# Optimization experiments

Hardware: AMD Instinct MI355X
Metric: run time of the kernel (lower is better)

## Reference

```python
import jax, jax.numpy as jnp
import numpy as np

ITERATIONS = 20  # Resonator(iterations=20)
B, F, V, D = 128, 4, 2048, 4096


def _hardsign(x):
    # bipolar normalization used by MAP-VSA multiset(normalize=True); ties -> +1
    return jnp.where(x >= 0, 1.0, -1.0).astype(x.dtype)


def setup_inputs() -> dict:
    key = jax.random.key(0)
    k1, k2 = jax.random.split(key, 2)
    # bipolar codebooks: (F, V, D)
    codebooks = _hardsign(jax.random.normal(k1, (F, V, D), dtype=jnp.float32))
    # a realistic composite input: bind (elementwise product) of one codevector per factor
    idx = jax.random.randint(k2, (B, F), 0, V)                       # (B, F)
    chosen = codebooks[jnp.arange(F)[None, :], idx]                  # (B, F, D)
    inputs = jnp.prod(chosen, axis=1)                                # (B, D)
    # standard resonator init: normalized superposition of each codebook
    init_estimates = jnp.broadcast_to(
        _hardsign(jnp.sum(codebooks, axis=1)), (B, F, D)
    ).astype(jnp.float32)                                            # (B, F, D)
    return {"inputs": inputs, "init_estimates": init_estimates, "codebooks": codebooks}


def _resonator_step(inputs, est, codebooks):
    # est: (B, F, D). rolled stack over k=1..F-1 -> (B, F, F-1, D)
    f = est.shape[-2]
    rolled = jnp.stack([jnp.roll(est, k, axis=-2) for k in range(1, f)], axis=-2)
    inv_others = jnp.prod(rolled, axis=-2)          # multibind over dim -2 -> (B, F, D)
    new_est = inputs[:, None, :] * inv_others       # bind -> (B, F, D)
    sim = jnp.einsum('bfd,fvd->bfv', new_est, codebooks)   # similarity (activation='NONE')
    # multiset(codebooks, sim, normalize=True)
    return _hardsign(jnp.einsum('bfv,fvd->bfd', sim, codebooks))


def reference(inputs, init_estimates, codebooks):
    def body(carry, i):
        est, k, done = carry
        new = _resonator_step(inputs, est, codebooks)
        eq = jnp.all(new == est)          # convergence check (fixed point)
        k = jnp.where(done, k, i)
        return (new, k, done | eq), None

    carry0 = (init_estimates, jnp.int32(0), jnp.bool_(False))
    (est, k, _), _ = jax.lax.scan(body, carry0, jnp.arange(ITERATIONS, dtype=jnp.int32))
    # cleanup: argmax of |similarity| per factor (argmax_abs=True)
    sim = jnp.einsum('bfd,fvd->bfv', est, codebooks)
    outcome = jnp.argmax(jnp.abs(sim), axis=-1)     # (B, F) int indices
    return outcome, k
```

## Files before the change

### kernel.cpp

```cpp
#include <hip/hip_runtime.h>
#include <stdint.h>

#define B_    128
#define F_    4
#define V_    2048
#define D_    4096
#define DW    64
#define VW    32
#define ITERS 20
#define NKT   16
#define NBLK  512
#define ESLOT (B_ * F_ * DW)
#define SSLOT ((size_t)F_ * B_ * V_)

typedef _Float16 half8 __attribute__((ext_vector_type(8)));
typedef float   floatx4 __attribute__((ext_vector_type(4)));

__device__ __forceinline__ void cstore64(uint64_t* p, uint64_t v) {
    __hip_atomic_store(p, v, __ATOMIC_RELAXED, __HIP_MEMORY_SCOPE_AGENT);
}
__device__ __forceinline__ void cstore32(uint32_t* p, uint32_t v) {
    __hip_atomic_store(p, v, __ATOMIC_RELAXED, __HIP_MEMORY_SCOPE_AGENT);
}

__device__ __forceinline__ void xbar(int* bar, int gen) {
    __syncthreads();
    if (threadIdx.x == 0) {
        int s = blockIdx.x & 15;
        int t = __hip_atomic_fetch_add(&bar[s * 16], 1, __ATOMIC_RELAXED,
                                       __HIP_MEMORY_SCOPE_AGENT);
        if (t == gen * (NBLK / 16) - 1)
            __hip_atomic_fetch_add(&bar[256], 1, __ATOMIC_RELAXED,
                                   __HIP_MEMORY_SCOPE_AGENT);
        int spins = 0;
        while (__hip_atomic_load(&bar[256], __ATOMIC_RELAXED,
                                 __HIP_MEMORY_SCOPE_AGENT) < gen * 16) {
            __builtin_amdgcn_s_sleep(2);
            if (++spins > (1 << 16)) break;
        }
    }
    __syncthreads();
}

__device__ __forceinline__ void pack16(const float* __restrict__ x,
                                       uint64_t* __restrict__ bits, int t) {
    const float4* p = (const float4*)x + (size_t)t * 4;
    uint32_t m = 0;
    #pragma unroll
    for (int j = 0; j < 4; ++j) {
        float4 v = p[j];
        m |= (__float_as_uint(v.x) >> 31) << (4 * j + 0);
        m |= (__float_as_uint(v.y) >> 31) << (4 * j + 1);
        m |= (__float_as_uint(v.z) >> 31) << (4 * j + 2);
        m |= (__float_as_uint(v.w) >> 31) << (4 * j + 3);
    }
    ((unsigned short*)bits)[t] = (unsigned short)m;
}

__global__ __launch_bounds__(256) void k_setup(
        const float* __restrict__ cb, const float* __restrict__ inite,
        const float* __restrict__ inputs,
        uint64_t* __restrict__ cb_bits, uint64_t* __restrict__ est0,
        uint64_t* __restrict__ in_bits,
        int* __restrict__ flags, int* __restrict__ keys) {
    int gtid = blockIdx.x * 256 + threadIdx.x;
    const int T = 512 * 256;
    const int ncb = (F_ * V_ * D_) / 16;
    for (int t = gtid; t < ncb; t += T) pack16(cb, cb_bits, t);
    pack16(inite, est0, gtid);
    if (gtid < (B_ * D_) / 16) pack16(inputs, in_bits, gtid);
    if (gtid < 32) flags[gtid] = 0;
    if (gtid < B_ * F_) keys[gtid] = 0;
}

__global__ void k_packT(const uint64_t* __restrict__ cb_bits,
                        uint64_t* __restrict__ cbT) {
    int vw = blockIdx.x, dwg = blockIdx.y, f = blockIdx.z;
    int lane = threadIdx.x & 63;
    int dw = dwg * 4 + (threadIdx.x >> 6);
    uint64_t w = cb_bits[((size_t)f * V_ + vw * 64 + lane) * DW + dw];
    uint64_t r = 0;
    for (int d2 = 0; d2 < 64; ++d2) {
        uint64_t m = __ballot((unsigned)((w >> d2) & 1));
        if (lane == d2) r = m;
    }
    cbT[((size_t)f * D_ + dw * 64 + lane) * VW + vw] = r;
}

__global__ __launch_bounds__(256, 2) void k_loop(
        const uint64_t* __restrict__ cb_bits, const uint64_t* __restrict__ cbT,
        uint64_t* __restrict__ est_base, const uint64_t* __restrict__ in_bits,
        _Float16* __restrict__ simf_base, int* __restrict__ flags, int* bar) {
    const int bid = blockIdx.x;
    const int tid = threadIdx.x;
    int g = 0;

    __shared__ __align__(16) unsigned char LDSU[49152];
    __shared__ int bd;

    #pragma unroll 1
    for (int i = 0; i < ITERS; ++i) {
        const uint64_t* esti = est_base + (size_t)i * ESLOT;
        uint64_t*       esto = est_base + (size_t)(i + 1) * ESLOT;
        _Float16*       simf = simf_base + (size_t)i * SSLOT;

        {
            int vt = bid & 31, bt = (bid >> 5) & 3, f = bid >> 7;
            int v0 = vt * 64, b0 = bt * 32;
            ulonglong2* CB2 = (ulonglong2*)LDSU;
            ulonglong2* NB2 = (ulonglong2*)(LDSU + 32768);
            #pragma unroll
            for (int it = 0; it < 8; ++it) {
                int cq = it * 256 + tid;
                int r = cq >> 5, ch = cq & 31;
                const ulonglong2* src = (const ulonglong2*)(cb_bits + ((size_t)f * V_ + v0 + r) * DW);
                CB2[r * 32 + (ch ^ (r & 7))] = src[ch];
            }
            #pragma unroll
            for (int it = 0; it < 4; ++it) {
                int cq = it * 256 + tid;
                int r = cq >> 5, ch = cq & 31;
                int b = b0 + r;
                const ulonglong2* iv = (const ulonglong2*)(in_bits + (size_t)b * DW);
                const uint64_t* eb = esti + (size_t)b * F_ * DW;
                ulonglong2 i2 = iv[ch];
                ulonglong2 e0 = ((const ulonglong2*)(eb + 0 * DW))[ch];
                ulonglong2 e1 = ((const ulonglong2*)(eb + 1 * DW))[ch];
                ulonglong2 e2 = ((const ulonglong2*)(eb + 2 * DW))[ch];
                ulonglong2 e3 = ((const ulonglong2*)(eb + 3 * DW))[ch];
                uint64_t ex = (f == 0) ? e0.x : (f == 1) ? e1.x : (f == 2) ? e2.x : e3.x;
                uint64_t ey = (f == 0) ? e0.y : (f == 1) ? e1.y : (f == 2) ? e2.y : e3.y;
                ulonglong2 val;
                val.x = i2.x ^ e0.x ^ e1.x ^ e2.x ^ e3.x ^ ex;
                val.y = i2.y ^ e0.y ^ e1.y ^ e2.y ^ e3.y ^ ey;
                NB2[r * 32 + (ch ^ (r & 7))] = val;
            }
            __syncthreads();

            int vv = tid & 15, bb = tid >> 4;
            int svz = vv & 7, sbz = bb & 7;
            int pc[2][4];
            #pragma unroll
            for (int j = 0; j < 2; ++j)
                #pragma unroll
                for (int ii = 0; ii < 4; ++ii) pc[j][ii] = 0;

            #pragma unroll 4
            for (int ch = 0; ch < 32; ++ch) {
                ulonglong2 c[4], n[2];
                #pragma unroll
                for (int ii = 0; ii < 4; ++ii)
                    c[ii] = CB2[(vv + 16 * ii) * 32 + (ch ^ svz)];
                #pragma unroll
                for (int j = 0; j < 2; ++j)
                    n[j] = NB2[(bb + 16 * j) * 32 + (ch ^ sbz)];
                #pragma unroll
                for (int j = 0; j < 2; ++j)
                    #pragma unroll
                    for (int ii = 0; ii < 4; ++ii)
                        pc[j][ii] += __popcll(n[j].x ^ c[ii].x) + __popcll(n[j].y ^ c[ii].y);
            }
            #pragma unroll
            for (int j = 0; j < 2; ++j) {
                int b = b0 + bb + 16 * j;
                #pragma unroll
                for (int ii = 0; ii < 4; ++ii) {
                    int v = v0 + vv + 16 * ii;
                    union { _Float16 hf; unsigned short us; } cv;
                    cv.hf = (_Float16)(2048 - pc[j][ii]);
                    int other = __shfl_xor((int)cv.us, 1, 64);
                    if (!(vv & 1)) {
                        uint32_t packv = (uint32_t)cv.us | ((uint32_t)other << 16);
                        cstore32((uint32_t*)&simf[((size_t)f * B_ + b) * V_ + v], packv);
                    }
                }
            }
        }
        xbar(bar, ++g);

        {
            int gnt = bid & 63, gmt = (bid >> 6) & 1, gf = bid >> 7;
            int m0 = gmt * 64, n0 = gnt * 64;
            int lane = tid & 63, wave = tid >> 6;
            int lrow = lane & 15, lq = lane >> 4;
            int wm = wave & 1, wn = wave >> 1;

            uint64_t* Bb = (uint64_t*)LDSU;
            _Float16* As = (_Float16*)(LDSU + 16384);
            if (tid == 0) bd = 0;

            const uint64_t* bsrc = cbT + ((size_t)gf * D_ + n0) * VW;
            #pragma unroll
            for (int p = 0; p < 4; ++p) {
                int chunk = p * 256 + tid;
                int dloc = chunk >> 4, cw = chunk & 15;
                ulonglong2 val = *(const ulonglong2*)&bsrc[dloc * VW + cw * 2];
                *(ulonglong2*)&Bb[dloc * VW + ((cw ^ (dloc & 15)) * 2)] = val;
            }

            const _Float16* Ab = simf + (size_t)gf * B_ * V_ + (size_t)m0 * V_;
            int arow = tid >> 4, acol = tid & 15;
            half8 areg[4];
            #pragma unroll
            for (int p = 0; p < 4; ++p)
                areg[p] = *(const half8*)&Ab[(size_t)(p * 16 + arow) * V_ + acol * 8];

            floatx4 acc[2][2] = {};

            const uint64_t SPREAD = 0x1000200040008000ull;
            const uint64_t SMASK  = 0x8000800080008000ull;
            const uint64_t PONE   = 0x3C003C003C003C00ull;

            #pragma unroll 1
            for (int kt = 0; kt < NKT; ++kt) {
                __syncthreads();
                #pragma unroll
                for (int p = 0; p < 4; ++p)
                    *(half8*)&As[(p * 16 + arow) * 128 + ((acol ^ arow) * 8)] = areg[p];
                if (kt + 1 < NKT) {
                    #pragma unroll
                    for (int p = 0; p < 4; ++p)
                        areg[p] = *(const half8*)&Ab[(size_t)(p * 16 + arow) * V_ + (kt + 1) * 128 + acol * 8];
                }
                __syncthreads();

                ulonglong2 bw[2];
                #pragma unroll
                for (int nt2 = 0; nt2 < 2; ++nt2) {
                    int dloc = wn * 32 + nt2 * 16 + lrow;
                    bw[nt2] = *(const ulonglong2*)&Bb[dloc * VW + ((kt ^ (dloc & 15)) * 2)];
                }
                #pragma unroll
                for (int ks = 0; ks < 4; ++ks) {
                    half8 af[2];
                    #pragma unroll
                    for (int mt2 = 0; mt2 < 2; ++mt2) {
                        int row = wm * 32 + mt2 * 16 + lrow;
                        af[mt2] = *(const half8*)&As[row * 128 + (((ks * 4 + lq) ^ lrow) * 8)];
                    }
                    half8 bfrag[2];
                    #pragma unroll
                    for (int nt2 = 0; nt2 < 2; ++nt2) {
                        uint64_t w = (ks < 2) ? bw[nt2].x : bw[nt2].y;
                        uint32_t byte = (uint32_t)(w >> ((((ks & 1) * 4 + lq)) * 8)) & 0xFFu;
                        union { uint64_t q[2]; half8 h; } bu;
                        bu.q[0] = (((uint64_t)(byte & 0xFu) * SPREAD) & SMASK) ^ PONE;
                        bu.q[1] = (((uint64_t)(byte >> 4)   * SPREAD) & SMASK) ^ PONE;
                        bfrag[nt2] = bu.h;
                    }
                    #pragma unroll
                    for (int mt2 = 0; mt2 < 2; ++mt2)
                        #pragma unroll
                        for (int nt2 = 0; nt2 < 2; ++nt2)
                            acc[mt2][nt2] = __builtin_amdgcn_mfma_f32_16x16x32_f16(
                                af[mt2], bfrag[nt2], acc[mt2][nt2], 0, 0, 0);
                }
            }

            __syncthreads();
            unsigned char* S = (unsigned char*)As;
            #pragma unroll
            for (int mt2 = 0; mt2 < 2; ++mt2)
                #pragma unroll
                for (int nt2 = 0; nt2 < 2; ++nt2)
                    #pragma unroll
                    for (int r = 0; r < 4; ++r) {
                        int row = wm * 32 + mt2 * 16 + lq * 4 + r;
                        int col = wn * 32 + nt2 * 16 + lrow;
                        S[row * 64 + col] = (acc[mt2][nt2][r] < 0.0f) ? 1 : 0;
                    }
            __syncthreads();
            if (tid < 64) {
                const uint64_t* Sw = (const uint64_t*)S;
                uint64_t m = 0;
                #pragma unroll
                for (int j = 0; j < 8; ++j) {
                    uint64_t w = Sw[tid * 8 + j];
                    m |= ((w * 0x0102040810204080ull) >> 56) << (8 * j);
                }
                size_t widx = ((size_t)(m0 + tid) * F_ + gf) * DW + gnt;
                uint64_t old = esti[widx];
                cstore64(&esto[widx], m);
                if (old != m) atomicOr(&bd, 1);
            }
            __syncthreads();
            if (tid == 0 && bd) atomicOr(&flags[i], 1);
        }
        if (i + 1 < ITERS) xbar(bar, ++g);
    }
}

__global__ __launch_bounds__(256) void k_argmax(
        const uint64_t* __restrict__ cb_bits,
        const uint64_t* __restrict__ est_bits,
        int* __restrict__ keys) {
    int vt = blockIdx.x, f = blockIdx.y;
    int v0 = vt * 32;
    int tid = threadIdx.x;

    __shared__ __align__(16) ulonglong2 EB2[128 * 32];
    __shared__ __align__(16) ulonglong2 CBa[32 * 32];

    #pragma unroll
    for (int it = 0; it < 16; ++it) {
        int cq = it * 256 + tid;
        int r = cq >> 5, ch = cq & 31;
        const ulonglong2* src = (const ulonglong2*)(est_bits + ((size_t)r * F_ + f) * DW);
        EB2[r * 32 + (ch ^ (r & 7))] = src[ch];
    }
    #pragma unroll
    for (int it = 0; it < 4; ++it) {
        int cq = it * 256 + tid;
        int r = cq >> 5, ch = cq & 31;
        const ulonglong2* src = (const ulonglong2*)(cb_bits + ((size_t)f * V_ + v0 + r) * DW);
        CBa[r * 32 + (ch ^ (r & 7))] = src[ch];
    }
    __syncthreads();

    int vv = tid & 15, bb = tid >> 4;
    int svz = vv & 7, sbz = bb & 7;
    int pc[8][2];
    #pragma unroll
    for (int j = 0; j < 8; ++j) { pc[j][0] = 0; pc[j][1] = 0; }

    #pragma unroll 4
    for (int ch = 0; ch < 32; ++ch) {
        ulonglong2 c[2], n[8];
        #pragma unroll
        for (int i = 0; i < 2; ++i)
            c[i] = CBa[(vv + 16 * i) * 32 + (ch ^ svz)];
        #pragma unroll
        for (int j = 0; j < 8; ++j)
            n[j] = EB2[(bb + 16 * j) * 32 + (ch ^ sbz)];
        #pragma unroll
        for (int j = 0; j < 8; ++j)
            #pragma unroll
            for (int i = 0; i < 2; ++i)
                pc[j][i] += __popcll(n[j].x ^ c[i].x) + __popcll(n[j].y ^ c[i].y);
    }

    #pragma unroll
    for (int j = 0; j < 8; ++j) {
        int kj = (int)0x80000000;
        #pragma unroll
        for (int i = 0; i < 2; ++i) {
            int v = v0 + vv + 16 * i;
            int m = 2048 - pc[j][i]; if (m < 0) m = -m;
            int key = (m << 11) | (2047 - v);
            if (key > kj) kj = key;
        }
        #pragma unroll
        for (int s = 1; s < 16; s <<= 1) {
            int o = __shfl_xor(kj, s, 64);
            if (o > kj) kj = o;
        }
        if ((tid & 15) == 0)
            atomicMax(&keys[(size_t)(bb + 16 * j) * F_ + f], kj);
    }
}

__global__ void k_final(const int* __restrict__ keys, const int* __restrict__ flags,
                        int* __restrict__ out) {
    int tid = blockIdx.x * blockDim.x + threadIdx.x;
    if (tid < B_ * F_) out[tid] = 2047 - (keys[tid] & 0x7FF);
    if (tid == 0) {
        int k = ITERS - 1;
        for (int i = 0; i < ITERS; ++i) if (flags[i] == 0) { k = i; break; }
        out[B_ * F_] = k;
    }
}

extern "C" void kernel_launch(void* const* d_in, const int* in_sizes, int n_in,
                              void* d_out, int out_size, void* d_ws, size_t ws_size,
                              hipStream_t stream) {
    const float* inputs = (const float*)d_in[0];
    const float* inite  = (const float*)d_in[1];
    const float* cb     = (const float*)d_in[2];
    int* out = (int*)d_out;

    char* ws = (char*)d_ws;
    uint64_t* cb_bits  = (uint64_t*)ws;  ws += (size_t)F_ * V_ * DW * 8;
    uint64_t* cbT_bits = (uint64_t*)ws;  ws += (size_t)F_ * D_ * VW * 8;
    uint64_t* est_base = (uint64_t*)ws;  ws += (size_t)(ITERS + 1) * ESLOT * 8;
    uint64_t* in_bits  = (uint64_t*)ws;  ws += (size_t)B_ * DW * 8;
    _Float16* simf     = (_Float16*)ws;  ws += (size_t)ITERS * SSLOT * 2;
    int*      flags    = (int*)ws;       ws += 32 * 4;
    int*      keys     = (int*)ws;       ws += B_ * F_ * 4;
    int*      bar      = (int*)ws;       ws += 2048;

    hipMemsetAsync(bar, 0, 2048, stream);

    k_setup<<<512, 256, 0, stream>>>(cb, inite, inputs, cb_bits, est_base,
                                     in_bits, flags, keys);
    k_packT<<<dim3(32, 16, 4), 256, 0, stream>>>(cb_bits, cbT_bits);
    k_loop<<<NBLK, 256, 0, stream>>>(cb_bits, cbT_bits, est_base, in_bits,
                                     simf, flags, bar);
    k_argmax<<<dim3(64, 4), 256, 0, stream>>>(cb_bits,
                                              est_base + (size_t)ITERS * ESLOT, keys);
    k_final<<<2, 256, 0, stream>>>(keys, flags, out);
}
```

Measured before the change: 924.5 us.

## Keep codebook tiles resident in LDS across iterations and remap block indices

Loads each block's similarity-phase codebook tile and transposed-codebook GEMM tile into LDS once before the iteration loop instead of reloading them every iteration. LDS grows to 64 KB so both tiles stay resident alongside the per-iteration buffers. Block-to-tile mapping is also reshuffled so the low bits of the block index spread across factor and batch tiles, which changes which XCD/L2 each tile lands on. The larger LDS footprint may reduce occupancy below two blocks per CU.

Result: faster. 902.1 us (-2.4%).

```diff
diff --git a/kernel.cpp b/kernel.cpp
--- a/kernel.cpp
+++ b/kernel.cpp
@@ -95,8 +95,47 @@
     const int tid = threadIdx.x;
     int g = 0;
 
-    __shared__ __align__(16) unsigned char LDSU[49152];
+    __shared__ __align__(16) unsigned char LDSU[65536];
     __shared__ int bd;
+
+    const int sgrp = bid & 7;
+    const int s_bt = sgrp & 3, s_fhi = sgrp >> 2;
+    const int shi  = bid >> 3;
+    const int s_vt = shi & 31, s_flo = shi >> 5;
+    const int s_f  = s_fhi + 2 * s_flo;
+    const int s_v0 = s_vt * 64, s_b0 = s_bt * 32;
+
+    const int ggrp = bid & 7;
+    const int g_mt = ggrp & 1, g_f = ggrp >> 1;
+    const int g_nt = bid >> 3;
+    const int g_m0 = g_mt * 64, g_n0 = g_nt * 64;
+
+    ulonglong2* CB2 = (ulonglong2*)LDSU;
+    ulonglong2* NB2 = (ulonglong2*)(LDSU + 32768);
+    _Float16*   As  = (_Float16*)(LDSU + 32768);
+    uint64_t*   Bb  = (uint64_t*)(LDSU + 49152);
+
+    #pragma unroll
+    for (int it = 0; it < 8; ++it) {
+        int cq = it * 256 + tid;
+        int r = cq >> 5, ch = cq & 31;
+        const ulonglong2* src = (const ulonglong2*)(cb_bits + ((size_t)s_f * V_ + s_v0 + r) * DW);
+        CB2[r * 32 + (ch ^ (r & 7))] = src[ch];
+    }
+    {
+        const uint64_t* bsrc = cbT + ((size_t)g_f * D_ + g_n0) * VW;
+        #pragma unroll
+        for (int p = 0; p < 4; ++p) {
+            int chunk = p * 256 + tid;
+            int dloc = chunk >> 4, cw = chunk & 15;
+            ulonglong2 val = *(const ulonglong2*)&bsrc[dloc * VW + cw * 2];
+            *(ulonglong2*)&Bb[dloc * VW + ((cw ^ (dloc & 15)) * 2)] = val;
+        }
+    }
+
+    const uint64_t SPREAD = 0x1000200040008000ull;
+    const uint64_t SMASK  = 0x8000800080008000ull;
+    const uint64_t PONE   = 0x3C003C003C003C00ull;
 
     #pragma unroll 1
     for (int i = 0; i < ITERS; ++i) {
@@ -105,22 +144,11 @@
         _Float16*       simf = simf_base + (size_t)i * SSLOT;
 
         {
-            int vt = bid & 31, bt = (bid >> 5) & 3, f = bid >> 7;
-            int v0 = vt * 64, b0 = bt * 32;
-            ulonglong2* CB2 = (ulonglong2*)LDSU;
-            ulonglong2* NB2 = (ulonglong2*)(LDSU + 32768);
-            #pragma unroll
-            for (int it = 0; it < 8; ++it) {
-                int cq = it * 256 + tid;
-                int r = cq >> 5, ch = cq & 31;
-                const ulonglong2* src = (const ulonglong2*)(cb_bits + ((size_t)f * V_ + v0 + r) * DW);
-                CB2[r * 32 + (ch ^ (r & 7))] = src[ch];
-            }
             #pragma unroll
             for (int it = 0; it < 4; ++it) {
                 int cq = it * 256 + tid;
                 int r = cq >> 5, ch = cq & 31;
-                int b = b0 + r;
+                int b = s_b0 + r;
                 const ulonglong2* iv = (const ulonglong2*)(in_bits + (size_t)b * DW);
                 const uint64_t* eb = esti + (size_t)b * F_ * DW;
                 ulonglong2 i2 = iv[ch];
@@ -128,8 +156,8 @@
                 ulonglong2 e1 = ((const ulonglong2*)(eb + 1 * DW))[ch];
                 ulonglong2 e2 = ((const ulonglong2*)(eb + 2 * DW))[ch];
                 ulonglong2 e3 = ((const ulonglong2*)(eb + 3 * DW))[ch];
-                uint64_t ex = (f == 0) ? e0.x : (f == 1) ? e1.x : (f == 2) ? e2.x : e3.x;
-                uint64_t ey = (f == 0) ? e0.y : (f == 1) ? e1.y : (f == 2) ? e2.y : e3.y;
+                uint64_t ex = (s_f == 0) ? e0.x : (s_f == 1) ? e1.x : (s_f == 2) ? e2.x : e3.x;
+                uint64_t ey = (s_f == 0) ? e0.y : (s_f == 1) ? e1.y : (s_f == 2) ? e2.y : e3.y;
                 ulonglong2 val;
                 val.x = i2.x ^ e0.x ^ e1.x ^ e2.x ^ e3.x ^ ex;
                 val.y = i2.y ^ e0.y ^ e1.y ^ e2.y ^ e3.y ^ ey;
@@ -162,16 +190,16 @@
             }
             #pragma unroll
             for (int j = 0; j < 2; ++j) {
-                int b = b0 + bb + 16 * j;
+                int b = s_b0 + bb + 16 * j;
                 #pragma unroll
                 for (int ii = 0; ii < 4; ++ii) {
-                    int v = v0 + vv + 16 * ii;
+                    int v = s_v0 + vv + 16 * ii;
                     union { _Float16 hf; unsigned short us; } cv;
                     cv.hf = (_Float16)(2048 - pc[j][ii]);
                     int other = __shfl_xor((int)cv.us, 1, 64);
                     if (!(vv & 1)) {
                         uint32_t packv = (uint32_t)cv.us | ((uint32_t)other << 16);
-                        cstore32((uint32_t*)&simf[((size_t)f * B_ + b) * V_ + v], packv);
+                        cstore32((uint32_t*)&simf[((size_t)s_f * B_ + b) * V_ + v], packv);
                     }
                 }
             }
@@ -179,26 +207,12 @@
         xbar(bar, ++g);
 
         {
-            int gnt = bid & 63, gmt = (bid >> 6) & 1, gf = bid >> 7;
-            int m0 = gmt * 64, n0 = gnt * 64;
             int lane = tid & 63, wave = tid >> 6;
             int lrow = lane & 15, lq = lane >> 4;
             int wm = wave & 1, wn = wave >> 1;
-
-            uint64_t* Bb = (uint64_t*)LDSU;
-            _Float16* As = (_Float16*)(LDSU + 16384);
             if (tid == 0) bd = 0;
 
-            const uint64_t* bsrc = cbT + ((size_t)gf * D_ + n0) * VW;
-            #pragma unroll
-            for (int p = 0; p < 4; ++p) {
-                int chunk = p * 256 + tid;
-                int dloc = chunk >> 4, cw = chunk & 15;
-                ulonglong2 val = *(const ulonglong2*)&bsrc[dloc * VW + cw * 2];
-                *(ulonglong2*)&Bb[dloc * VW + ((cw ^ (dloc & 15)) * 2)] = val;
-            }
-
-            const _Float16* Ab = simf + (size_t)gf * B_ * V_ + (size_t)m0 * V_;
+            const _Float16* Ab = simf + (size_t)g_f * B_ * V_ + (size_t)g_m0 * V_;
             int arow = tid >> 4, acol = tid & 15;
             half8 areg[4];
             #pragma unroll
@@ -206,10 +220,6 @@
                 areg[p] = *(const half8*)&Ab[(size_t)(p * 16 + arow) * V_ + acol * 8];
 
             floatx4 acc[2][2] = {};
-
-            const uint64_t SPREAD = 0x1000200040008000ull;
-            const uint64_t SMASK  = 0x8000800080008000ull;
-            const uint64_t PONE   = 0x3C003C003C003C00ull;
 
             #pragma unroll 1
             for (int kt = 0; kt < NKT; ++kt) {
@@ -278,7 +288,7 @@
                     uint64_t w = Sw[tid * 8 + j];
                     m |= ((w * 0x0102040810204080ull) >> 56) << (8 * j);
                 }
-                size_t widx = ((size_t)(m0 + tid) * F_ + gf) * DW + gnt;
+                size_t widx = ((size_t)(g_m0 + tid) * F_ + g_f) * DW + g_nt;
                 uint64_t old = esti[widx];
                 cstore64(&esto[widx], m);
                 if (old != m) atomicOr(&bd, 1);
```
